# Performance work log

Hardware: AMD Instinct MI355X
Metric: run time of the kernel (lower is better)

## Reference

```python
import jax, jax.numpy as jnp
import numpy as np

B, S, D, H, F = 4, 2048, 1024, 16, 4096
DK = D // H
EPS = 1e-5


def layer_norm(x, gamma, beta):
    mu = jnp.mean(x, axis=-1, keepdims=True)
    var = jnp.mean(jnp.square(x - mu), axis=-1, keepdims=True)
    return (x - mu) * jax.lax.rsqrt(var + EPS) * gamma + beta


def setup_inputs() -> dict:
    key = jax.random.key(0)
    ks = jax.random.split(key, 16)
    s = 1.0 / np.sqrt(D)
    sf = 1.0 / np.sqrt(F)
    inp = {
        "x": jax.random.normal(ks[0], (B, S, D), dtype=jnp.float32),
        # causal mask: 0 = blocked, 1 = visible (masked_fill(mask == 0, -1e9))
        "mask": jnp.tril(jnp.ones((S, S), dtype=jnp.int32))[None, None],
        "Wq": jax.random.normal(ks[1], (D, D), dtype=jnp.float32) * s,
        "bq": jnp.zeros((D,), dtype=jnp.float32),
        "Wk": jax.random.normal(ks[2], (D, D), dtype=jnp.float32) * s,
        "bk": jnp.zeros((D,), dtype=jnp.float32),
        "Wv": jax.random.normal(ks[3], (D, D), dtype=jnp.float32) * s,
        "bv": jnp.zeros((D,), dtype=jnp.float32),
        "Wo": jax.random.normal(ks[4], (D, D), dtype=jnp.float32) * s,
        "bo": jnp.zeros((D,), dtype=jnp.float32),
        "g1": jnp.ones((D,), dtype=jnp.float32),
        "b1": jnp.zeros((D,), dtype=jnp.float32),
        "W1": jax.random.normal(ks[5], (D, F), dtype=jnp.float32) * s,
        "c1": jnp.zeros((F,), dtype=jnp.float32),
        "W2": jax.random.normal(ks[6], (F, D), dtype=jnp.float32) * sf,
        "c2": jnp.zeros((D,), dtype=jnp.float32),
        "g2": jnp.ones((D,), dtype=jnp.float32),
        "b2": jnp.zeros((D,), dtype=jnp.float32),
    }
    return inp


def reference(x, mask, Wq, bq, Wk, bk, Wv, bv, Wo, bo, g1, b1, W1, c1, W2, c2, g2, b2):
    b = x.shape[0]
    # qkv projections -> [B, H, S, DK]
    q = (x @ Wq + bq).reshape(b, S, H, DK).transpose(0, 2, 1, 3)
    k = (x @ Wk + bk).reshape(b, S, H, DK).transpose(0, 2, 1, 3)
    v = (x @ Wv + bv).reshape(b, S, H, DK).transpose(0, 2, 1, 3)
    scores = jnp.einsum("bhqd,bhkd->bhqk", q, k) / np.sqrt(DK)
    scores = jnp.where(mask == 0, -1e9, scores)
    attn = jax.nn.softmax(scores, axis=-1)
    out = jnp.einsum("bhqk,bhkd->bhqd", attn, v)
    out = out.transpose(0, 2, 1, 3).reshape(b, S, D)
    attended = out @ Wo + bo
    x = layer_norm(x + attended, g1, b1)
    ff = jax.nn.relu(x @ W1 + c1) @ W2 + c2
    x = layer_norm(x + ff, g2, b2)
    return x
```

## Files before the change

### kernel.cpp

```cpp
#include <hip/hip_runtime.h>
#include <cstdint>
#include <cstddef>

#define DEV __device__ __forceinline__

typedef unsigned short u16;
typedef __attribute__((ext_vector_type(8))) short bf16x8;
typedef __attribute__((ext_vector_type(8))) u16  u16x8;
typedef __attribute__((ext_vector_type(4))) float f32x4;

constexpr int Bn = 4, Sn = 2048, Dn = 1024, Hn = 16, Fn = 4096, DKn = 64;
constexpr int Mn = Bn * Sn;

DEV u16 f2b(float f) {
    unsigned u = __float_as_uint(f);
    unsigned r = (u + 0x7fffu + ((u >> 16) & 1u)) >> 16;
    return (u16)r;
}
DEV float b2f(u16 h) { return __uint_as_float(((unsigned)h) << 16); }

typedef __attribute__((address_space(1))) void gvoid;
typedef __attribute__((address_space(3))) void lvoid;
DEV void gl_lds16(const u16* g, u16* l) {
    __builtin_amdgcn_global_load_lds((gvoid*)g, (lvoid*)l, 16, 0, 0);
}

DEV f32x4 mfma16(bf16x8 a, bf16x8 b, f32x4 c) {
    return __builtin_amdgcn_mfma_f32_16x16x32_bf16(a, b, c, 0, 0, 0);
}

__global__ __launch_bounds__(256) void cvt_f32_bf16(const float* __restrict__ in,
                                                    u16* __restrict__ out) {
    size_t i = ((size_t)blockIdx.x * 256 + threadIdx.x) * 8;
    float4 a = *(const float4*)(in + i);
    float4 b = *(const float4*)(in + i + 4);
    u16x8 o;
    o[0] = f2b(a.x); o[1] = f2b(a.y); o[2] = f2b(a.z); o[3] = f2b(a.w);
    o[4] = f2b(b.x); o[5] = f2b(b.y); o[6] = f2b(b.z); o[7] = f2b(b.w);
    *(u16x8*)(out + i) = o;
}

__global__ __launch_bounds__(256) void transpose_cvt(const float* __restrict__ W,
                                                     u16* __restrict__ Wt, int K, int N) {
    __shared__ float tile[32][33];
    int n0 = blockIdx.x * 32, k0 = blockIdx.y * 32;
    int tx = threadIdx.x, ty = threadIdx.y;
    for (int r = ty; r < 32; r += 8) tile[r][tx] = W[(size_t)(k0 + r) * N + n0 + tx];
    __syncthreads();
    for (int r = ty; r < 32; r += 8) Wt[(size_t)(n0 + r) * K + k0 + tx] = f2b(tile[tx][r]);
}

__global__ __launch_bounds__(256) void vt_kernel(const u16* __restrict__ V,
                                                 u16* __restrict__ Vt) {
    __shared__ u16 t[32][34];
    int s0 = blockIdx.x * 32, d0 = blockIdx.y * 32, bh = blockIdx.z;
    int tx = threadIdx.x, ty = threadIdx.y;
    const u16* in = V + (size_t)bh * Sn * DKn;
    u16* out = Vt + (size_t)bh * DKn * Sn;
    for (int r = ty; r < 32; r += 8) t[r][tx] = in[(size_t)(s0 + r) * DKn + d0 + tx];
    __syncthreads();
    for (int r = ty; r < 32; r += 8) out[(size_t)(d0 + r) * Sn + s0 + tx] = t[tx][r];
}

template <int RELU, int RESID, int OUT_BF16, int QKV>
__global__ __launch_bounds__(256) void gemm_kernel(
    const u16* __restrict__ A, const u16* __restrict__ Bt,
    const float* __restrict__ bias, const float* __restrict__ biasB,
    const float* __restrict__ biasC,
    const float* __restrict__ residF, const u16* __restrict__ residB,
    float* __restrict__ Cf, u16* __restrict__ Cb,
    int M, int N, int K, float oscale) {
    constexpr int BK = 32;
    __shared__ __align__(16) u16 As[128 * BK];
    __shared__ __align__(16) u16 Bs[128 * BK];
    const int tid = threadIdx.x, wave = tid >> 6, lane = tid & 63;
    const int quad = lane >> 4, l16 = lane & 15;
    const int row0 = blockIdx.x * 128, col0 = blockIdx.y * 128;
    const int wm = wave & 1, wn = wave >> 1;

    f32x4 acc[4][4];
    for (int mt = 0; mt < 4; mt++)
        for (int nt = 0; nt < 4; nt++)
            acc[mt][nt] = f32x4{0.f, 0.f, 0.f, 0.f};

    const int srow = lane >> 2, scol = (lane & 3) * 8;
    const u16* Ag = A + (size_t)(row0 + wave * 16 + srow) * K + scol;
    const u16* Bg = Bt + (size_t)(col0 + wave * 16 + srow) * K + scol;
    u16* AsW = As + (wave * 16) * BK;
    u16* BsW = Bs + (wave * 16) * BK;

    for (int k0 = 0; k0 < K; k0 += BK) {
        __syncthreads();
        gl_lds16(Ag + k0, AsW);
        gl_lds16(Ag + (size_t)64 * K + k0, AsW + 64 * BK);
        gl_lds16(Bg + k0, BsW);
        gl_lds16(Bg + (size_t)64 * K + k0, BsW + 64 * BK);
        __syncthreads();

        bf16x8 af[4], bfr[4];
        for (int mt = 0; mt < 4; mt++)
            af[mt] = *(const bf16x8*)(As + (wm * 64 + mt * 16 + l16) * BK + quad * 8);
        for (int nt = 0; nt < 4; nt++)
            bfr[nt] = *(const bf16x8*)(Bs + (wn * 64 + nt * 16 + l16) * BK + quad * 8);
        for (int mt = 0; mt < 4; mt++)
            for (int nt = 0; nt < 4; nt++)
                acc[mt][nt] = mfma16(af[mt], bfr[nt], acc[mt][nt]);
    }

    int g = 0; const float* bp = bias; float osc = 1.0f;
    if (QKV == 2) {
        g = (col0 >> 10);
        bp = (g == 0) ? bias : ((g == 1) ? biasB : biasC);
        osc = (g == 0) ? oscale : 1.0f;
    }

    for (int nt = 0; nt < 4; nt++) {
        int col = col0 + wn * 64 + nt * 16 + l16;
        int cc = col & 1023;
        float bv = (QKV == 2) ? bp[cc] : bias[col];
        for (int mt = 0; mt < 4; mt++) {
            int rbase = row0 + wm * 64 + mt * 16 + quad * 4;
            for (int r = 0; r < 4; r++) {
                int row = rbase + r;
                float v = acc[mt][nt][r] + bv;
                if (RELU) v = fmaxf(v, 0.f);
                if (RESID == 1) v += residF[(size_t)row * N + col];
                if (RESID == 2) v += b2f(residB[(size_t)row * N + col]);
                if (QKV == 2) {
                    int bb = row >> 11, s = row & 2047, h = cc >> 6, dk = cc & 63;
                    Cb[(size_t)g * Mn * Dn +
                       ((size_t)(bb * Hn + h) * Sn + s) * DKn + dk] = f2b(v * osc);
                } else if (OUT_BF16) {
                    Cb[(size_t)row * N + col] = f2b(v);
                } else {
                    Cf[(size_t)row * N + col] = v;
                }
            }
        }
    }
}

__global__ __launch_bounds__(256, 4) void attn4_kernel(const u16* __restrict__ Q,
                                                       const u16* __restrict__ K,
                                                       const u16* __restrict__ Vt,
                                                       u16* __restrict__ O) {
    __shared__ __align__(16) u16 Ks[128 * 64];
    __shared__ __align__(16) u16 Vs[64 * 128];
    int tid = threadIdx.x, wave = tid >> 6, lane = tid & 63;
    int quad = lane >> 4, l16 = lane & 15;
    int bh = blockIdx.y, b = bh >> 4, h = bh & 15;
    int p = blockIdx.x;
    const u16* Qh = Q + (size_t)bh * Sn * DKn;
    const u16* Kh = K + (size_t)bh * Sn * DKn;
    const u16* Vh = Vt + (size_t)bh * DKn * Sn;
    u16* Pw = Ks + wave * 16 * 128;

    const int ksr = wave * 32 + (lane >> 3), ksb = lane & 7;
    const int vsr = wave * 16 + (lane >> 4), vsb = lane & 15;

    for (int t = 0; t < 2; t++) {
        int qt = t ? p : 31 - p;
        int R0 = qt * 64 + wave * 16;

        bf16x8 qf[2];
        for (int h2 = 0; h2 < 2; h2++)
            qf[h2] = *(const bf16x8*)(Qh + (size_t)(R0 + l16) * DKn + h2 * 32 + quad * 8);

        float m_i[4], l_i[4];
        f32x4 accO[4];
        for (int r = 0; r < 4; r++) { m_i[r] = -1e30f; l_i[r] = 0.f; }
        for (int nt = 0; nt < 4; nt++) accO[nt] = f32x4{0.f, 0.f, 0.f, 0.f};

        int n2 = (qt + 2) >> 1;
        for (int kt2 = 0; kt2 < n2; kt2++) {
            __syncthreads();
            for (int i = 0; i < 4; i++) {
                int rk = ksr + i * 8;
                gl_lds16(Kh + (size_t)(kt2 * 128 + rk) * DKn + ((ksb ^ (rk & 7)) * 8),
                         Ks + (wave * 32 + i * 8) * 64);
                int rv = vsr + i * 4;
                gl_lds16(Vh + (size_t)rv * Sn + kt2 * 128 + ((vsb ^ (rv & 7)) * 8),
                         Vs + (wave * 16 + i * 4) * 128);
            }
            __syncthreads();

            f32x4 sc[8];
            for (int nt = 0; nt < 8; nt++) sc[nt] = f32x4{0.f, 0.f, 0.f, 0.f};
            for (int h2 = 0; h2 < 2; h2++)
                for (int nt = 0; nt < 8; nt++) {
                    bf16x8 kf = *(const bf16x8*)(Ks + (nt * 16 + l16) * 64 +
                                                 (((h2 * 4 + quad) ^ (l16 & 7)) * 8));
                    sc[nt] = mfma16(qf[h2], kf, sc[nt]);
                }
            __syncthreads();

            if (kt2 == n2 - 1) {
                int crow = R0 + quad * 4 - kt2 * 128;
                for (int r = 0; r < 4; r++)
                    for (int nt = 0; nt < 8; nt++)
                        if (nt * 16 + l16 > crow + r) sc[nt][r] = -1e30f;
            }

            for (int r = 0; r < 4; r++) {
                float mx = sc[0][r];
                for (int nt = 1; nt < 8; nt++) mx = fmaxf(mx, sc[nt][r]);
                for (int off = 1; off < 16; off <<= 1) mx = fmaxf(mx, __shfl_xor(mx, off, 64));
                float mn = fmaxf(m_i[r], mx);
                float al = exp2f(m_i[r] - mn);
                m_i[r] = mn;
                float ps = 0.f;
                for (int nt = 0; nt < 8; nt++) {
                    float pv = exp2f(sc[nt][r] - mn);
                    sc[nt][r] = pv;
                    ps += pv;
                }
                l_i[r] = l_i[r] * al + ps;
                for (int nt = 0; nt < 4; nt++) accO[nt][r] *= al;
            }

            for (int r = 0; r < 4; r++)
                for (int nt = 0; nt < 8; nt++)
                    Pw[(quad * 4 + r) * 128 + nt * 16 + l16] = f2b(sc[nt][r]);
            for (int c = 0; c < 4; c++) {
                bf16x8 pf = *(const bf16x8*)(Pw + l16 * 128 + c * 32 + quad * 8);
                for (int nt = 0; nt < 4; nt++) {
                    bf16x8 vf = *(const bf16x8*)(Vs + (nt * 16 + l16) * 128 +
                                                 (((c * 4 + quad) ^ (l16 & 7)) * 8));
                    accO[nt] = mfma16(pf, vf, accO[nt]);
                }
            }
        }

        for (int r = 0; r < 4; r++) {
            float lr = l_i[r];
            for (int off = 1; off < 16; off <<= 1) lr += __shfl_xor(lr, off, 64);
            float inv = 1.f / lr;
            int sg = R0 + quad * 4 + r;
            for (int nt = 0; nt < 4; nt++)
                O[((size_t)b * Sn + sg) * Dn + h * DKn + nt * 16 + l16] = f2b(accO[nt][r] * inv);
        }
    }
}

template <int OUT_BF16>
__global__ __launch_bounds__(256) void ln_kernel(const float* __restrict__ in,
                                                 const float* __restrict__ gamma,
                                                 const float* __restrict__ beta,
                                                 float* __restrict__ outF,
                                                 u16* __restrict__ outB) {
    int row = blockIdx.x, tid = threadIdx.x;
    float4 v = ((const float4*)(in + (size_t)row * Dn))[tid];
    float s = v.x + v.y + v.z + v.w;
    float q = v.x * v.x + v.y * v.y + v.z * v.z + v.w * v.w;
    for (int off = 32; off >= 1; off >>= 1) {
        s += __shfl_xor(s, off, 64);
        q += __shfl_xor(q, off, 64);
    }
    __shared__ float rs[4], rq[4];
    int wave = tid >> 6, lane = tid & 63;
    if (lane == 0) { rs[wave] = s; rq[wave] = q; }
    __syncthreads();
    s = rs[0] + rs[1] + rs[2] + rs[3];
    q = rq[0] + rq[1] + rq[2] + rq[3];
    float mu = s * (1.f / Dn);
    float rstd = rsqrtf(q * (1.f / Dn) - mu * mu + 1e-5f);
    float4 g = ((const float4*)gamma)[tid];
    float4 be = ((const float4*)beta)[tid];
    float o0 = (v.x - mu) * rstd * g.x + be.x;
    float o1 = (v.y - mu) * rstd * g.y + be.y;
    float o2 = (v.z - mu) * rstd * g.z + be.z;
    float o3 = (v.w - mu) * rstd * g.w + be.w;
    if (OUT_BF16) {
        ushort4 u;
        u.x = f2b(o0); u.y = f2b(o1); u.z = f2b(o2); u.w = f2b(o3);
        ((ushort4*)outB)[(size_t)row * (Dn / 4) + tid] = u;
    } else {
        ((float4*)outF)[(size_t)row * (Dn / 4) + tid] = make_float4(o0, o1, o2, o3);
    }
}

extern "C" void kernel_launch(void* const* d_in, const int* in_sizes, int n_in,
                              void* d_out, int out_size, void* d_ws, size_t ws_size,
                              hipStream_t stream) {
    const float* x  = (const float*)d_in[0];
    const float* Wq = (const float*)d_in[2];  const float* bq = (const float*)d_in[3];
    const float* Wk = (const float*)d_in[4];  const float* bk = (const float*)d_in[5];
    const float* Wv = (const float*)d_in[6];  const float* bv = (const float*)d_in[7];
    const float* Wo = (const float*)d_in[8];  const float* bo = (const float*)d_in[9];
    const float* g1 = (const float*)d_in[10]; const float* b1 = (const float*)d_in[11];
    const float* W1 = (const float*)d_in[12]; const float* c1 = (const float*)d_in[13];
    const float* W2 = (const float*)d_in[14]; const float* c2 = (const float*)d_in[15];
    const float* g2 = (const float*)d_in[16]; const float* b2 = (const float*)d_in[17];

    char* ws = (char*)d_ws;
    const size_t MB = 1ull << 20;
    u16*   Xb  = (u16*)(ws + 0 * MB);
    u16*   WqT = (u16*)(ws + 16 * MB);
    u16*   WkT = (u16*)(ws + 18 * MB);
    u16*   WvT = (u16*)(ws + 20 * MB);
    u16*   WoT = (u16*)(ws + 22 * MB);
    u16*   W1T = (u16*)(ws + 24 * MB);
    u16*   W2T = (u16*)(ws + 32 * MB);
    u16*   Qb  = (u16*)(ws + 40 * MB);
    u16*   Kb  = (u16*)(ws + 56 * MB);
    u16*   Vb  = (u16*)(ws + 72 * MB);
    u16*   Ob  = (u16*)(ws + 88 * MB);
    u16*   Vt  = (u16*)(ws + 104 * MB);
    float* h1  = (float*)(ws + 104 * MB);
    u16*   ff1 = (u16*)(ws + 136 * MB);
    u16*   ln1b = Qb;
    float* h2   = h1;

    const float qscale = 0.125f * 1.44269504f;

    dim3 tb(32, 8);
    cvt_f32_bf16<<<dim3(Mn * Dn / (256 * 8)), 256, 0, stream>>>(x, Xb);
    transpose_cvt<<<dim3(Dn / 32, Dn / 32), tb, 0, stream>>>(Wq, WqT, Dn, Dn);
    transpose_cvt<<<dim3(Dn / 32, Dn / 32), tb, 0, stream>>>(Wk, WkT, Dn, Dn);
    transpose_cvt<<<dim3(Dn / 32, Dn / 32), tb, 0, stream>>>(Wv, WvT, Dn, Dn);
    transpose_cvt<<<dim3(Dn / 32, Dn / 32), tb, 0, stream>>>(Wo, WoT, Dn, Dn);
    transpose_cvt<<<dim3(Fn / 32, Dn / 32), tb, 0, stream>>>(W1, W1T, Dn, Fn);
    transpose_cvt<<<dim3(Dn / 32, Fn / 32), tb, 0, stream>>>(W2, W2T, Fn, Dn);

    gemm_kernel<0, 0, 1, 2><<<dim3(Mn / 128, 3 * Dn / 128), 256, 0, stream>>>(
        Xb, WqT, bq, bk, bv, nullptr, nullptr, nullptr, Qb, Mn, 3 * Dn, Dn, qscale);

    vt_kernel<<<dim3(Sn / 32, DKn / 32, Bn * Hn), tb, 0, stream>>>(Vb, Vt);

    attn4_kernel<<<dim3(16, Bn * Hn), 256, 0, stream>>>(Qb, Kb, Vt, Ob);

    gemm_kernel<0, 1, 0, 0><<<dim3(Mn / 128, Dn / 128), 256, 0, stream>>>(
        Ob, WoT, bo, nullptr, nullptr, x, nullptr, h1, nullptr, Mn, Dn, Dn, 1.0f);
    ln_kernel<1><<<Mn, 256, 0, stream>>>(h1, g1, b1, nullptr, ln1b);

    gemm_kernel<1, 0, 1, 0><<<dim3(Mn / 128, Fn / 128), 256, 0, stream>>>(
        ln1b, W1T, c1, nullptr, nullptr, nullptr, nullptr, nullptr, ff1, Mn, Fn, Dn, 1.0f);
    gemm_kernel<0, 2, 0, 0><<<dim3(Mn / 128, Dn / 128), 256, 0, stream>>>(
        ff1, W2T, c2, nullptr, nullptr, nullptr, ln1b, h2, nullptr, Mn, Dn, Fn, 1.0f);
    ln_kernel<0><<<Mn, 256, 0, stream>>>(h2, g2, b2, (float*)d_out, nullptr);
}
```

Measured before the change: 608.0 us.

## Compute transposed scores so P stays in registers for the PV MFMA

Attention now computes S^T by swapping the MFMA operands (K as A, Q as B). Each lane then holds the score column for a single query row, which reduces the softmax row reductions to two cross-quad shuffles. P feeds the PV product directly from registers through the 16x16x16 bf16 MFMA, removing the LDS round-trip for P and its barrier. K is now loaded straight from global memory into registers instead of being staged in LDS, which frees shared memory but exposes global load latency inside the loop. Output stores become 4-wide vectors.

```diff
diff --git a/kernel.cpp b/kernel.cpp
--- a/kernel.cpp
+++ b/kernel.cpp
@@ -6,6 +6,7 @@
 
 typedef unsigned short u16;
 typedef __attribute__((ext_vector_type(8))) short bf16x8;
+typedef __attribute__((ext_vector_type(4))) short s16x4;
 typedef __attribute__((ext_vector_type(8))) u16  u16x8;
 typedef __attribute__((ext_vector_type(4))) float f32x4;
 
@@ -27,6 +28,10 @@
 
 DEV f32x4 mfma16(bf16x8 a, bf16x8 b, f32x4 c) {
     return __builtin_amdgcn_mfma_f32_16x16x32_bf16(a, b, c, 0, 0, 0);
+}
+
+DEV f32x4 mfma_pv(s16x4 a, s16x4 b, f32x4 c) {
+    return __builtin_amdgcn_mfma_f32_16x16x16bf16_1k(a, b, c, 0, 0, 0);
 }
 
 __global__ __launch_bounds__(256) void cvt_f32_bf16(const float* __restrict__ in,
@@ -140,11 +145,10 @@
     }
 }
 
-__global__ __launch_bounds__(256, 4) void attn4_kernel(const u16* __restrict__ Q,
+__global__ __launch_bounds__(256, 4) void attn5_kernel(const u16* __restrict__ Q,
                                                        const u16* __restrict__ K,
                                                        const u16* __restrict__ Vt,
                                                        u16* __restrict__ O) {
-    __shared__ __align__(16) u16 Ks[128 * 64];
     __shared__ __align__(16) u16 Vs[64 * 128];
     int tid = threadIdx.x, wave = tid >> 6, lane = tid & 63;
     int quad = lane >> 4, l16 = lane & 15;
@@ -153,91 +157,98 @@
     const u16* Qh = Q + (size_t)bh * Sn * DKn;
     const u16* Kh = K + (size_t)bh * Sn * DKn;
     const u16* Vh = Vt + (size_t)bh * DKn * Sn;
-    u16* Pw = Ks + wave * 16 * 128;
-
-    const int ksr = wave * 32 + (lane >> 3), ksb = lane & 7;
-    const int vsr = wave * 16 + (lane >> 4), vsb = lane & 15;
 
     for (int t = 0; t < 2; t++) {
         int qt = t ? p : 31 - p;
-        int R0 = qt * 64 + wave * 16;
+        int R0w = qt * 64 + wave * 16;
+        int qg = R0w + l16;
 
         bf16x8 qf[2];
         for (int h2 = 0; h2 < 2; h2++)
-            qf[h2] = *(const bf16x8*)(Qh + (size_t)(R0 + l16) * DKn + h2 * 32 + quad * 8);
-
-        float m_i[4], l_i[4];
+            qf[h2] = *(const bf16x8*)(Qh + (size_t)qg * DKn + h2 * 32 + quad * 8);
+
+        float m_i = -1e30f, l_i = 0.f;
         f32x4 accO[4];
-        for (int r = 0; r < 4; r++) { m_i[r] = -1e30f; l_i[r] = 0.f; }
-        for (int nt = 0; nt < 4; nt++) accO[nt] = f32x4{0.f, 0.f, 0.f, 0.f};
+        for (int dt = 0; dt < 4; dt++) accO[dt] = f32x4{0.f, 0.f, 0.f, 0.f};
 
         int n2 = (qt + 2) >> 1;
         for (int kt2 = 0; kt2 < n2; kt2++) {
+            const u16* Kp = Kh + (size_t)kt2 * 128 * DKn;
+
+            bf16x8 kf[8];
+            for (int nt = 0; nt < 8; nt++)
+                kf[nt] = *(const bf16x8*)(Kp + (size_t)(nt * 16 + l16) * DKn + quad * 8);
+
             __syncthreads();
             for (int i = 0; i < 4; i++) {
-                int rk = ksr + i * 8;
-                gl_lds16(Kh + (size_t)(kt2 * 128 + rk) * DKn + ((ksb ^ (rk & 7)) * 8),
-                         Ks + (wave * 32 + i * 8) * 64);
-                int rv = vsr + i * 4;
-                gl_lds16(Vh + (size_t)rv * Sn + kt2 * 128 + ((vsb ^ (rv & 7)) * 8),
+                int rv = wave * 16 + i * 4 + (lane >> 4);
+                int gb = (lane & 15) ^ (rv & 7);
+                gl_lds16(Vh + (size_t)rv * Sn + kt2 * 128 + gb * 8,
                          Vs + (wave * 16 + i * 4) * 128);
             }
             __syncthreads();
 
             f32x4 sc[8];
-            for (int nt = 0; nt < 8; nt++) sc[nt] = f32x4{0.f, 0.f, 0.f, 0.f};
-            for (int h2 = 0; h2 < 2; h2++)
-                for (int nt = 0; nt < 8; nt++) {
-                    bf16x8 kf = *(const bf16x8*)(Ks + (nt * 16 + l16) * 64 +
-                                                 (((h2 * 4 + quad) ^ (l16 & 7)) * 8));
-                    sc[nt] = mfma16(qf[h2], kf, sc[nt]);
-                }
-            __syncthreads();
+            for (int nt = 0; nt < 8; nt++)
+                sc[nt] = mfma16(kf[nt], qf[0], f32x4{0.f, 0.f, 0.f, 0.f});
+            for (int nt = 0; nt < 8; nt++)
+                kf[nt] = *(const bf16x8*)(Kp + (size_t)(nt * 16 + l16) * DKn + 32 + quad * 8);
+            for (int nt = 0; nt < 8; nt++)
+                sc[nt] = mfma16(kf[nt], qf[1], sc[nt]);
 
             if (kt2 == n2 - 1) {
-                int crow = R0 + quad * 4 - kt2 * 128;
-                for (int r = 0; r < 4; r++)
-                    for (int nt = 0; nt < 8; nt++)
-                        if (nt * 16 + l16 > crow + r) sc[nt][r] = -1e30f;
+                int kb = kt2 * 128 + quad * 4;
+                for (int nt = 0; nt < 8; nt++)
+                    for (int r = 0; r < 4; r++)
+                        if (kb + nt * 16 + r > qg) sc[nt][r] = -1e30f;
             }
 
-            for (int r = 0; r < 4; r++) {
-                float mx = sc[0][r];
-                for (int nt = 1; nt < 8; nt++) mx = fmaxf(mx, sc[nt][r]);
-                for (int off = 1; off < 16; off <<= 1) mx = fmaxf(mx, __shfl_xor(mx, off, 64));
-                float mn = fmaxf(m_i[r], mx);
-                float al = exp2f(m_i[r] - mn);
-                m_i[r] = mn;
-                float ps = 0.f;
-                for (int nt = 0; nt < 8; nt++) {
+            float mx = sc[0][0];
+            for (int nt = 0; nt < 8; nt++)
+                for (int r = 0; r < 4; r++) mx = fmaxf(mx, sc[nt][r]);
+            mx = fmaxf(mx, __shfl_xor(mx, 16, 64));
+            mx = fmaxf(mx, __shfl_xor(mx, 32, 64));
+            float mn = fmaxf(m_i, mx);
+            float al = exp2f(m_i - mn);
+            m_i = mn;
+            float ps = 0.f;
+            for (int nt = 0; nt < 8; nt++)
+                for (int r = 0; r < 4; r++) {
                     float pv = exp2f(sc[nt][r] - mn);
                     sc[nt][r] = pv;
                     ps += pv;
                 }
-                l_i[r] = l_i[r] * al + ps;
-                for (int nt = 0; nt < 4; nt++) accO[nt][r] *= al;
-            }
-
-            for (int r = 0; r < 4; r++)
-                for (int nt = 0; nt < 8; nt++)
-                    Pw[(quad * 4 + r) * 128 + nt * 16 + l16] = f2b(sc[nt][r]);
-            for (int c = 0; c < 4; c++) {
-                bf16x8 pf = *(const bf16x8*)(Pw + l16 * 128 + c * 32 + quad * 8);
-                for (int nt = 0; nt < 4; nt++) {
-                    bf16x8 vf = *(const bf16x8*)(Vs + (nt * 16 + l16) * 128 +
-                                                 (((c * 4 + quad) ^ (l16 & 7)) * 8));
-                    accO[nt] = mfma16(pf, vf, accO[nt]);
+            l_i = l_i * al + ps;
+            for (int dt = 0; dt < 4; dt++)
+                for (int r = 0; r < 4; r++) accO[dt][r] *= al;
+
+            for (int nt = 0; nt < 8; nt++) {
+                s16x4 pb;
+                pb[0] = (short)f2b(sc[nt][0]);
+                pb[1] = (short)f2b(sc[nt][1]);
+                pb[2] = (short)f2b(sc[nt][2]);
+                pb[3] = (short)f2b(sc[nt][3]);
+                int slot = (nt * 2 + (quad >> 1)) ^ (l16 & 7);
+                int off = slot * 8 + (quad & 1) * 4;
+                for (int dt = 0; dt < 4; dt++) {
+                    s16x4 vf = *(const s16x4*)(Vs + (dt * 16 + l16) * 128 + off);
+                    accO[dt] = mfma_pv(vf, pb, accO[dt]);
                 }
             }
         }
 
-        for (int r = 0; r < 4; r++) {
-            float lr = l_i[r];
-            for (int off = 1; off < 16; off <<= 1) lr += __shfl_xor(lr, off, 64);
-            float inv = 1.f / lr;
-            int sg = R0 + quad * 4 + r;
-            for (int nt = 0; nt < 4; nt++)
-                O[((size_t)b * Sn + sg) * Dn + h * DKn + nt * 16 + l16] = f2b(accO[nt][r] * inv);
+        float lr = l_i;
+        lr += __shfl_xor(lr, 16, 64);
+        lr += __shfl_xor(lr, 32, 64);
+        float inv = 1.f / lr;
+        u16* Op = O + ((size_t)b * Sn + qg) * Dn + h * DKn + quad * 4;
+        for (int dt = 0; dt < 4; dt++) {
+            ushort4 o;
+            o.x = f2b(accO[dt][0] * inv);
+            o.y = f2b(accO[dt][1] * inv);
+            o.z = f2b(accO[dt][2] * inv);
+            o.w = f2b(accO[dt][3] * inv);
+            *(ushort4*)(Op + dt * 16) = o;
         }
     }
 }
@@ -327,7 +338,7 @@
 
     vt_kernel<<<dim3(Sn / 32, DKn / 32, Bn * Hn), tb, 0, stream>>>(Vb, Vt);
 
-    attn4_kernel<<<dim3(16, Bn * Hn), 256, 0, stream>>>(Qb, Kb, Vt, Ob);
+    attn5_kernel<<<dim3(16, Bn * Hn), 256, 0, stream>>>(Qb, Kb, Vt, Ob);
 
     gemm_kernel<0, 1, 0, 0><<<dim3(Mn / 128, Dn / 128), 256, 0, stream>>>(
         Ob, WoT, bo, nullptr, nullptr, x, nullptr, h1, nullptr, Mn, Dn, Dn, 1.0f);
```

Measured after the change: 679.5 us. +11.8%, slower.
